# Optimization experiments

Hardware: AMD Instinct MI355X
Metric: run time of the kernel (lower is better)

## Reference

```python
import jax, jax.numpy as jnp
import numpy as np

T, B, S = 64, 128, 128
H = 200   # hidden_size
E = 200   # embedding_size
A = 100   # attention projection width
V = 10003 # vocab_size


def setup_inputs() -> dict:
    key = jax.random.key(0)
    ks = jax.random.split(key, 20)
    def n(k, shape, scale):
        return (jax.random.normal(k, shape, jnp.float32) * scale).astype(jnp.float32)
    return {
        "tokens": jax.random.randint(ks[0], (T, B), 0, V),
        "hidden": n(ks[1], (1, B, H), 0.1),
        "encoder_outputs": n(ks[2], (S, B, H), 1.0),
        "emb": n(ks[3], (V, E), 0.05),
        "W1": n(ks[4], (A, H), 0.07), "b1": n(ks[5], (A,), 0.07),
        "W2": n(ks[6], (A, H), 0.07), "b2": n(ks[7], (A,), 0.07),
        "W3": n(ks[8], (A, E), 0.07), "b3": n(ks[9], (A,), 0.07),
        "attn_W": n(ks[10], (1, A), 0.1), "attn_b": n(ks[11], (1,), 0.1),
        "gru_Wih": n(ks[12], (3 * H, E + H), 0.05), "gru_Whh": n(ks[13], (3 * H, H), 0.05),
        "gru_bih": n(ks[14], (3 * H,), 0.05), "gru_bhh": n(ks[15], (3 * H,), 0.05),
        "out_W": n(ks[16], (V, H), 0.05), "out_b": n(ks[17], (V,), 0.05),
    }


def reference(tokens, hidden, encoder_outputs, emb, W1, b1, W2, b2, W3, b3,
              attn_W, attn_b, gru_Wih, gru_Whh, gru_bih, gru_bhh, out_W, out_b):
    # eval mode: dropout is identity
    enc = jnp.transpose(encoder_outputs, (1, 0, 2))   # [B, S, H]
    embedded = emb[tokens]                            # [T, B, E]
    ah3 = embedded @ W3.T + b3                        # [T, B, A] (precomputed, as in torch)
    ah2 = enc @ W2.T + b2                             # [B, S, A]
    h0 = hidden[0]                                    # [B, H]

    def step(h, xs):
        emb_t, ah3_t = xs                             # [B,E], [B,A]
        ah1 = h @ W1.T + b1                           # [B, A]
        e = jax.nn.relu(ah1[:, None, :] + ah2 + ah3_t[:, None, :])  # [B, S, A]
        logits = (e @ attn_W.T + attn_b)[..., 0]      # [B, S]
        a = jax.nn.softmax(logits, axis=1)            # [B, S]
        ctx = jnp.einsum('bs,bsh->bh', a, enc)        # [B, H]
        x = jnp.concatenate([emb_t, ctx], axis=1)     # [B, E+H]
        gi = x @ gru_Wih.T + gru_bih                  # [B, 3H]
        gh = h @ gru_Whh.T + gru_bhh                  # [B, 3H]
        ir, iz, in_ = jnp.split(gi, 3, axis=1)
        hr, hz, hn = jnp.split(gh, 3, axis=1)
        r = jax.nn.sigmoid(ir + hr)
        z = jax.nn.sigmoid(iz + hz)
        nn_ = jnp.tanh(in_ + r * hn)
        h_new = (1.0 - z) * nn_ + z * h               # [B, H]
        logp = jax.nn.log_softmax(h_new @ out_W.T + out_b, axis=1)  # [B, V]
        return h_new, (logp, a)

    h_last, (outputs, attns) = jax.lax.scan(step, h0, (embedded, ah3))
    # outputs [T,B,V]; hidden [1,B,H]; attentions [T,B,1,S] (torch's view(B,1,S) per step)
    return outputs, h_last[None], attns[:, :, None, :]
```

## Files before the change

### kernel.cpp

```cpp
#include <hip/hip_runtime.h>
#include <hip/hip_bf16.h>
#include <cmath>

constexpr int T_ = 64, B_ = 128, S_ = 128, H_ = 200, E_ = 200, A_ = 100, V_ = 10003;
constexpr int KP = 224;
constexpr int VP = 10240;
constexpr int MROWS = T_ * B_;
constexpr int NCB = VP / 256;
constexpr int G3 = 3 * H_;
constexpr int EH = E_ + H_;
constexpr int ELD = 136;
constexpr int AH2P = 104;
constexpr int NP = 768;
constexpr int NP2 = 128;
constexpr int NTH = 512;
constexpr int NPK = 32;

typedef __attribute__((ext_vector_type(8))) short bf16x8;
typedef __attribute__((ext_vector_type(4))) float f32x4;
typedef __attribute__((ext_vector_type(2))) _Float16 h2;
typedef __attribute__((ext_vector_type(8))) _Float16 h8;

#if __has_builtin(__builtin_amdgcn_fdot2)
__device__ __forceinline__ float fdot2f(h2 a, h2 b, float c) {
  return __builtin_amdgcn_fdot2(a, b, c, false);
}
#else
__device__ __forceinline__ float fdot2f(h2 a, h2 b, float c) {
  return c + (float)a[0] * (float)b[0] + (float)a[1] * (float)b[1];
}
#endif

__device__ __forceinline__ float dot200p5(const h8* __restrict__ w, int stride,
                                          const h8* __restrict__ x) {
  const h8* p = w;
  h8 w0 = p[0]; p += stride;
  h8 w1 = p[0]; p += stride;
  h8 w2 = p[0]; p += stride;
  h8 w3 = p[0]; p += stride;
  h8 w4 = p[0]; p += stride;
  float a0 = 0.f, a1 = 0.f, a2 = 0.f, a3 = 0.f;
#define DOT_CONSUME(WREG, K)                    \
  {                                             \
    h8 xv = x[K];                               \
    h2 wp[4], xp[4];                            \
    __builtin_memcpy(wp, &WREG, 16);            \
    __builtin_memcpy(xp, &xv, 16);              \
    a0 = fdot2f(wp[0], xp[0], a0);              \
    a1 = fdot2f(wp[1], xp[1], a1);              \
    a2 = fdot2f(wp[2], xp[2], a2);              \
    a3 = fdot2f(wp[3], xp[3], a3);              \
  }
#define DOT_RELOAD(WREG) { WREG = p[0]; p += stride; }
  DOT_CONSUME(w0, 0)  DOT_RELOAD(w0)
  DOT_CONSUME(w1, 1)  DOT_RELOAD(w1)
  DOT_CONSUME(w2, 2)  DOT_RELOAD(w2)
  DOT_CONSUME(w3, 3)  DOT_RELOAD(w3)
  DOT_CONSUME(w4, 4)  DOT_RELOAD(w4)
  DOT_CONSUME(w0, 5)  DOT_RELOAD(w0)
  DOT_CONSUME(w1, 6)  DOT_RELOAD(w1)
  DOT_CONSUME(w2, 7)  DOT_RELOAD(w2)
  DOT_CONSUME(w3, 8)  DOT_RELOAD(w3)
  DOT_CONSUME(w4, 9)  DOT_RELOAD(w4)
  DOT_CONSUME(w0, 10) DOT_RELOAD(w0)
  DOT_CONSUME(w1, 11) DOT_RELOAD(w1)
  DOT_CONSUME(w2, 12) DOT_RELOAD(w2)
  DOT_CONSUME(w3, 13) DOT_RELOAD(w3)
  DOT_CONSUME(w4, 14) DOT_RELOAD(w4)
  DOT_CONSUME(w0, 15) DOT_RELOAD(w0)
  DOT_CONSUME(w1, 16) DOT_RELOAD(w1)
  DOT_CONSUME(w2, 17) DOT_RELOAD(w2)
  DOT_CONSUME(w3, 18) DOT_RELOAD(w3)
  DOT_CONSUME(w4, 19) DOT_RELOAD(w4)
  DOT_CONSUME(w0, 20)
  DOT_CONSUME(w1, 21)
  DOT_CONSUME(w2, 22)
  DOT_CONSUME(w3, 23)
  DOT_CONSUME(w4, 24)
#undef DOT_CONSUME
#undef DOT_RELOAD
  return (a0 + a1) + (a2 + a3);
}


__global__ __launch_bounds__(256) void k_pack(const float* __restrict__ W1,
                                              const float* __restrict__ Wih,
                                              const float* __restrict__ Whh,
                                              const float* __restrict__ W3,
                                              const float* __restrict__ W2,
                                              _Float16* __restrict__ W1h,
                                              _Float16* __restrict__ Wihh,
                                              _Float16* __restrict__ Whhh,
                                              __hip_bfloat16* __restrict__ wep,
                                              __hip_bfloat16* __restrict__ w2p,
                                              _Float16* __restrict__ ah2h) {
  const int stride = gridDim.x * blockDim.x;
  const int tid0 = blockIdx.x * blockDim.x + threadIdx.x;
  for (int idx = tid0; idx < 25 * A_ * 8; idx += stride) {
    int kk = idx & 7, a = (idx >> 3) % A_, k8 = idx / (8 * A_);
    W1h[idx] = (_Float16)W1[(size_t)a * H_ + k8 * 8 + kk];
  }
  for (int idx = tid0; idx < 50 * G3 * 8; idx += stride) {
    int kk = idx & 7, n = (idx >> 3) % G3, k8 = idx / (8 * G3);
    Wihh[idx] = (_Float16)Wih[(size_t)n * EH + k8 * 8 + kk];
  }
  for (int idx = tid0; idx < 25 * G3 * 8; idx += stride) {
    int kk = idx & 7, n = (idx >> 3) % G3, k8 = idx / (8 * G3);
    Whhh[idx] = (_Float16)Whh[(size_t)n * H_ + k8 * 8 + kk];
  }
  for (int idx = tid0; idx < (KP / 8) * NP * 8; idx += stride) {
    int kk = idx & 7, c = (idx >> 3) % NP, k8 = idx / (8 * NP);
    int k = k8 * 8 + kk;
    float v = 0.f;
    if (k < E_) {
      if (c < G3) v = Wih[(size_t)c * EH + k];
      else if (c < G3 + A_) v = W3[(size_t)(c - G3) * E_ + k];
    }
    wep[idx] = __float2bfloat16(v);
  }
  for (int idx = tid0; idx < (KP / 8) * NP2 * 8; idx += stride) {
    int kk = idx & 7, c = (idx >> 3) % NP2, k8 = idx / (8 * NP2);
    int k = k8 * 8 + kk;
    float v = (k < H_ && c < A_) ? W2[(size_t)c * H_ + k] : 0.f;
    w2p[idx] = __float2bfloat16(v);
  }
  for (int idx = tid0; idx < B_ * S_ * (AH2P - A_); idx += stride) {
    int row = idx / (AH2P - A_), col = A_ + idx % (AH2P - A_);
    ah2h[(size_t)row * AH2P + col] = (_Float16)0.f;
  }
}

__global__ __launch_bounds__(256) void k_genc(const float* __restrict__ encoder,
                                              const short* __restrict__ w2p,
                                              const float* __restrict__ b2,
                                              _Float16* __restrict__ ah2h) {
  constexpr int ALD = 232;
  __shared__ __align__(16) __hip_bfloat16 aL[128 * ALD];
  const int tid = threadIdx.x;
  const int w = tid >> 6, l = tid & 63, lm = l & 15, lg = l >> 4;
  const int r0 = blockIdx.y * 128;
  const int rloc = (w >> 1) * 64;
  const int v0 = (w & 1) * 64;

  for (int i = tid; i < 128 * KP; i += 256) {
    int row = i / KP, k = i - row * KP;
    float v = (k < H_) ? encoder[(size_t)(r0 + row) * H_ + k] : 0.f;
    aL[row * ALD + k] = __float2bfloat16(v);
  }
  __syncthreads();

  f32x4 acc[4][4] = {};
#pragma unroll
  for (int kt = 0; kt < KP / 32; ++kt) {
    const int k0 = kt * 32;
    bf16x8 af[4], bfr[4];
#pragma unroll
    for (int wm = 0; wm < 4; ++wm)
      af[wm] = *(const bf16x8*)(aL + (rloc + wm * 16 + lm) * ALD + k0 + lg * 8);
#pragma unroll
    for (int n = 0; n < 4; ++n)
      bfr[n] = *(const bf16x8*)(w2p + ((size_t)((k0 >> 3) + lg) * NP2 + v0 + n * 16 + lm) * 8);
#pragma unroll
    for (int wm = 0; wm < 4; ++wm)
#pragma unroll
      for (int n = 0; n < 4; ++n)
        acc[wm][n] = __builtin_amdgcn_mfma_f32_16x16x32_bf16(af[wm], bfr[n], acc[wm][n], 0, 0, 0);
  }

#pragma unroll
  for (int n = 0; n < 4; ++n) {
    const int vv = v0 + n * 16 + lm;
    if (vv >= A_) continue;
    const float bias = b2[vv];
#pragma unroll
    for (int wm = 0; wm < 4; ++wm) {
#pragma unroll
      for (int j = 0; j < 4; ++j) {
        const int grow = r0 + rloc + wm * 16 + lg * 4 + j;
        const int bb = grow & (B_ - 1);
        const int ss = grow >> 7;
        ah2h[((size_t)bb * S_ + ss) * AH2P + vv] = (_Float16)(acc[wm][n][j] + bias);
      }
    }
  }
}

__global__ __launch_bounds__(256) void k_gemb(const int* __restrict__ tokens,
                                              const float* __restrict__ emb,
                                              const short* __restrict__ wep,
                                              const float* __restrict__ bih,
                                              const float* __restrict__ b3,
                                              float* __restrict__ giX,
                                              float* __restrict__ ah3) {
  constexpr int ALD = 232;
  __shared__ __align__(16) __hip_bfloat16 aL[64 * ALD];
  __shared__ int tokL[64];
  const int tid = threadIdx.x;
  const int w = tid >> 6, l = tid & 63, lm = l & 15, lg = l >> 4;
  const int r0 = blockIdx.y * 64;
  const int v0 = blockIdx.x * 256 + w * 64;

  if (tid < 64) tokL[tid] = tokens[r0 + tid];
  __syncthreads();
  for (int i = tid; i < 64 * KP; i += 256) {
    int row = i / KP, k = i - row * KP;
    float v = (k < E_) ? emb[(size_t)tokL[row] * E_ + k] : 0.f;
    aL[row * ALD + k] = __float2bfloat16(v);
  }
  __syncthreads();

  f32x4 acc[4][4] = {};
#pragma unroll
  for (int kt = 0; kt < KP / 32; ++kt) {
    const int k0 = kt * 32;
    bf16x8 af[4], bfr[4];
#pragma unroll
    for (int wm = 0; wm < 4; ++wm)
      af[wm] = *(const bf16x8*)(aL + (wm * 16 + lm) * ALD + k0 + lg * 8);
#pragma unroll
    for (int n = 0; n < 4; ++n)
      bfr[n] = *(const bf16x8*)(wep + ((size_t)((k0 >> 3) + lg) * NP + v0 + n * 16 + lm) * 8);
#pragma unroll
    for (int wm = 0; wm < 4; ++wm)
#pragma unroll
      for (int n = 0; n < 4; ++n)
        acc[wm][n] = __builtin_amdgcn_mfma_f32_16x16x32_bf16(af[wm], bfr[n], acc[wm][n], 0, 0, 0);
  }

#pragma unroll
  for (int n = 0; n < 4; ++n) {
    const int vv = v0 + n * 16 + lm;
    const bool isGi = vv < G3;
    const bool isA3 = !isGi && vv < G3 + A_;
    const float bias = isGi ? bih[vv] : (isA3 ? b3[vv - G3] : 0.f);
#pragma unroll
    for (int wm = 0; wm < 4; ++wm) {
#pragma unroll
      for (int j = 0; j < 4; ++j) {
        const int row = r0 + wm * 16 + lg * 4 + j;
        const float val = acc[wm][n][j] + bias;
        if (isGi) giX[(size_t)row * G3 + vv] = val;
        else if (isA3) ah3[(size_t)row * A_ + (vv - G3)] = val;
      }
    }
  }
}

__global__ __launch_bounds__(NTH) void k_recur(const float* __restrict__ hidden0,
                                               const _Float16* __restrict__ ah2h,
                                               const float* __restrict__ ah3,
                                               const float* __restrict__ encoder,
                                               const _Float16* __restrict__ W1h,
                                               const float* __restrict__ b1,
                                               const float* __restrict__ attn_W,
                                               const float* __restrict__ attn_b,
                                               const _Float16* __restrict__ Wihh,
                                               const _Float16* __restrict__ Whhh,
                                               const float* __restrict__ bhh,
                                               const float* __restrict__ giX,
                                               const float* __restrict__ outW,
                                               __hip_bfloat16* __restrict__ wpk,
                                               __hip_bfloat16* __restrict__ hall,
                                               float* __restrict__ out_hidden,
                                               float* __restrict__ out_attn) {
  __shared__ __align__(16) _Float16 encLh[H_ * ELD];
  __shared__ __align__(16) h2 h16[100];
  __shared__ __align__(16) h2 xch[100];
  __shared__ __align__(16) h2 aLh[64];
  __shared__ float s1[AH2P];
  __shared__ float aW[AH2P];
  __shared__ float red[8];
  __shared__ float giL[G3];
  __shared__ float part[1200];

  const int b = blockIdx.x, tid = threadIdx.x;
  const int lane = tid & 63;

  if (b >= B_) {
    const int pt = (b - B_) * NTH + tid;
    const int pstride = NPK * NTH;
    const int total = (KP / 8) * VP * 8;
    for (int idx = pt; idx < total; idx += pstride) {
      int kk = idx & 7;
      int v = (idx >> 3) % VP;
      int kb = idx / (8 * VP);
      int k = kb * 8 + kk;
      float val = (k < H_ && v < V_) ? outW[(size_t)v * H_ + k] : 0.f;
      wpk[idx] = __float2bfloat16(val);
    }
    const __hip_bfloat16 z = __float2bfloat16(0.f);
    for (int idx = pt; idx < MROWS * (KP - H_); idx += pstride) {
      int row = idx / (KP - H_), col = H_ + idx % (KP - H_);
      hall[(size_t)row * KP + col] = z;
    }
    return;
  }

  for (int i = tid; i < S_ * H_; i += NTH) {
    int s = i / H_, h = i - s * H_;
    encLh[h * ELD + s] = (_Float16)encoder[((size_t)s * B_ + b) * H_ + h];
  }
  float hreg = 0.f, bhr = 0.f, bhz = 0.f, bhn = 0.f;
  if (tid < H_) {
    hreg = hidden0[b * H_ + tid];
    bhr = bhh[tid]; bhz = bhh[200 + tid]; bhn = bhh[400 + tid];
  }
  if (tid < 100) {
    h2 v;
    v[0] = (_Float16)hidden0[b * H_ + 2 * tid];
    v[1] = (_Float16)hidden0[b * H_ + 2 * tid + 1];
    h16[tid] = v;
  }
  for (int i = tid; i < AH2P; i += NTH) {
    aW[i] = (i < A_) ? attn_W[i] : 0.f;
    s1[i] = 0.f;
  }
  h8 ah2row[13];
  if (tid < S_) {
    const h8* src = (const h8*)(ah2h + ((size_t)b * S_ + tid) * AH2P);
#pragma unroll
    for (int r = 0; r < 13; ++r) ah2row[r] = src[r];
  }
  const float ab = attn_b[0];
  __syncthreads();

  const h8* W1h8 = (const h8*)W1h;
  const h8* Wihc8 = (const h8*)Wihh + (size_t)25 * G3;
  const h8* Whhh8 = (const h8*)Whhh;

  for (int t = 0; t < T_; ++t) {
    const h8* xs = (const h8*)h16;
    for (int u = tid; u < 700; u += NTH) {
      if (u < 100) {
        const float ah3A = ah3[((size_t)t * B_ + b) * A_ + u];
        const float b1A = b1[u];
        s1[u] = dot200p5(W1h8 + u, A_, xs) + b1A + ah3A;
      } else {
        const int g = u - 100;
        part[g] = dot200p5(Whhh8 + g, G3, xs);
      }
    }
    __syncthreads();

    float evw = 0.f;
    const int w01 = tid >> 6;
    if (tid < S_) {
      float acc = ab;
#pragma unroll
      for (int r = 0; r < 13; ++r) {
        h8 w = ah2row[r];
#pragma unroll
        for (int j = 0; j < 8; ++j) {
          const int a = r * 8 + j;
          acc += fmaxf(s1[a] + (float)w[j], 0.f) * aW[a];
        }
      }
      float m = acc;
#pragma unroll
      for (int off = 32; off > 0; off >>= 1) m = fmaxf(m, __shfl_xor(m, off, 64));
      evw = expf(acc - m);
      float sm = evw;
#pragma unroll
      for (int off = 32; off > 0; off >>= 1) sm += __shfl_xor(sm, off, 64);
      if (lane == 0) { red[w01] = m; red[4 + w01] = sm; }
    }
    __syncthreads();
    if (tid < S_) {
      const float m0 = red[0], m1 = red[1];
      const float M = fmaxf(m0, m1);
      const float SS = red[4] * expf(m0 - M) + red[5] * expf(m1 - M);
      const float av = evw * expf((w01 ? m1 : m0) - M) / SS;
      out_attn[((size_t)t * B_ + b) * S_ + tid] = av;
      const float avn = __shfl_xor(av, 1, 64);
      if ((tid & 1) == 0) {
        h2 v; v[0] = (_Float16)av; v[1] = (_Float16)avn;
        aLh[tid >> 1] = v;
      }
    }
    __syncthreads();

    if (tid < H_) {
      const h8* er = (const h8*)(encLh + tid * ELD);
      float c0 = 0.f, c1 = 0.f, c2 = 0.f, c3 = 0.f;
#pragma unroll
      for (int k8 = 0; k8 < 16; ++k8) {
        h8 evv = er[k8];
        h2 ep[4];
        __builtin_memcpy(ep, &evv, 16);
        c0 = fdot2f(ep[0], aLh[4 * k8 + 0], c0);
        c1 = fdot2f(ep[1], aLh[4 * k8 + 1], c1);
        c2 = fdot2f(ep[2], aLh[4 * k8 + 2], c2);
        c3 = fdot2f(ep[3], aLh[4 * k8 + 3], c3);
      }
      const float c = (c0 + c1) + (c2 + c3);
      const float cn = __shfl_xor(c, 1, 64);
      if ((tid & 1) == 0) {
        h2 v; v[0] = (_Float16)c; v[1] = (_Float16)cn;
        xch[tid >> 1] = v;
      }
    } else {
      const int j = tid - 200;
      if (j < 300) {
        float2 g2 = ((const float2*)(giX + ((size_t)t * B_ + b) * G3))[j];
        giL[2 * j] = g2.x;
        giL[2 * j + 1] = g2.y;
      }
    }
    __syncthreads();

    {
      const h8* xc8 = (const h8*)xch;
      for (int u = tid; u < 600; u += NTH) {
        part[600 + u] = dot200p5(Wihc8 + u, G3, xc8);
      }
    }
    __syncthreads();

    if (tid < H_) {
      const int n = tid;
      const float gir = giL[n] + part[600 + n];
      const float giz = giL[200 + n] + part[800 + n];
      const float gin = giL[400 + n] + part[1000 + n];
      const float ghr = part[n] + bhr;
      const float ghz = part[200 + n] + bhz;
      const float ghn = part[400 + n] + bhn;
      const float r = 1.f / (1.f + expf(-(gir + ghr)));
      const float z = 1.f / (1.f + expf(-(giz + ghz)));
      const float nn = tanhf(gin + r * ghn);
      const float hv = (1.f - z) * nn + z * hreg;
      hreg = hv;
      hall[((size_t)t * B_ + b) * KP + n] = __float2bfloat16(hv);
      const float hn2 = __shfl_xor(hv, 1, 64);
      if ((n & 1) == 0) {
        h2 v; v[0] = (_Float16)hv; v[1] = (_Float16)hn2;
        h16[n >> 1] = v;
      }
      if (t == T_ - 1) out_hidden[b * H_ + n] = hv;
    }
    __syncthreads();
  }
}

__global__ __launch_bounds__(256) void k_big0(const short* __restrict__ hb,
                                              const short* __restrict__ wpk,
                                              const float* __restrict__ outb,
                                              float* __restrict__ pmax,
                                              float* __restrict__ psum) {
  const int tid = threadIdx.x;
  const int w = tid >> 6, l = tid & 63;
  const int lm = l & 15, lg = l >> 4;
  const int r0 = blockIdx.y * 64;
  const int v0 = blockIdx.x * 256 + w * 64;

  f32x4 acc[4][4] = {};
#pragma unroll
  for (int kt = 0; kt < KP / 32; ++kt) {
    const int k0 = kt * 32;
    bf16x8 af[4], bfr[4];
#pragma unroll
    for (int wm = 0; wm < 4; ++wm)
      af[wm] = *(const bf16x8*)(hb + (size_t)(r0 + wm * 16 + lm) * KP + k0 + lg * 8);
#pragma unroll
    for (int n = 0; n < 4; ++n)
      bfr[n] = *(const bf16x8*)(wpk + ((size_t)((k0 >> 3) + lg) * VP + v0 + n * 16 + lm) * 8);
#pragma unroll
    for (int wm = 0; wm < 4; ++wm)
#pragma unroll
      for (int n = 0; n < 4; ++n)
        acc[wm][n] = __builtin_amdgcn_mfma_f32_16x16x32_bf16(af[wm], bfr[n], acc[wm][n], 0, 0, 0);
  }

  int vv[4]; float bias[4]; bool val[4];
#pragma unroll
  for (int n = 0; n < 4; ++n) {
    vv[n] = v0 + n * 16 + lm;
    val[n] = vv[n] < V_;
    bias[n] = val[n] ? outb[vv[n]] : 0.f;
  }

  __shared__ float smax[4][64], ssum[4][64];
#pragma unroll
  for (int wm = 0; wm < 4; ++wm) {
#pragma unroll
    for (int j = 0; j < 4; ++j) {
      float mv = -INFINITY;
#pragma unroll
      for (int n = 0; n < 4; ++n)
        if (val[n]) mv = fmaxf(mv, acc[wm][n][j] + bias[n]);
      for (int off = 8; off > 0; off >>= 1) mv = fmaxf(mv, __shfl_xor(mv, off, 64));
      float sv = 0.f;
#pragma unroll
      for (int n = 0; n < 4; ++n)
        if (val[n]) sv += expf(acc[wm][n][j] + bias[n] - mv);
      for (int off = 8; off > 0; off >>= 1) sv += __shfl_xor(sv, off, 64);
      if (lm == 0) {
        smax[w][wm * 16 + lg * 4 + j] = mv;
        ssum[w][wm * 16 + lg * 4 + j] = sv;
      }
    }
  }
  __syncthreads();
  if (tid < 64) {
    float mv = -INFINITY;
    for (int ww = 0; ww < 4; ++ww) mv = fmaxf(mv, smax[ww][tid]);
    float sv = 0.f;
    for (int ww = 0; ww < 4; ++ww) {
      float sw = ssum[ww][tid];
      if (sw > 0.f) sv += expf(smax[ww][tid] - mv) * sw;
    }
    pmax[(size_t)blockIdx.x * MROWS + r0 + tid] = mv;
    psum[(size_t)blockIdx.x * MROWS + r0 + tid] = sv;
  }
}

__global__ __launch_bounds__(256) void k_lse(const float* __restrict__ pmax,
                                             const float* __restrict__ psum,
                                             float* __restrict__ lse) {
  const int r = blockIdx.x * 256 + threadIdx.x;
  float mv = -INFINITY;
  for (int c = 0; c < NCB; ++c) mv = fmaxf(mv, pmax[(size_t)c * MROWS + r]);
  float sv = 0.f;
  for (int c = 0; c < NCB; ++c) {
    float sw = psum[(size_t)c * MROWS + r];
    if (sw > 0.f) sv += expf(pmax[(size_t)c * MROWS + r] - mv) * sw;
  }
  lse[r] = mv + logf(sv);
}

__global__ __launch_bounds__(256) void k_big1(const short* __restrict__ hb,
                                              const short* __restrict__ wpk,
                                              const float* __restrict__ outb,
                                              const float* __restrict__ lse,
                                              float* __restrict__ out_logp) {
  const int tid = threadIdx.x;
  const int w = tid >> 6, l = tid & 63;
  const int lm = l & 15, lg = l >> 4;
  const int r0 = blockIdx.y * 64;
  const int v0 = blockIdx.x * 256 + w * 64;

  __shared__ float lseL[64];
  if (tid < 64) lseL[tid] = lse[r0 + tid];

  f32x4 acc[4][4] = {};
#pragma unroll
  for (int kt = 0; kt < KP / 32; ++kt) {
    const int k0 = kt * 32;
    bf16x8 af[4], bfr[4];
#pragma unroll
    for (int wm = 0; wm < 4; ++wm)
      af[wm] = *(const bf16x8*)(hb + (size_t)(r0 + wm * 16 + lm) * KP + k0 + lg * 8);
#pragma unroll
    for (int n = 0; n < 4; ++n)
      bfr[n] = *(const bf16x8*)(wpk + ((size_t)((k0 >> 3) + lg) * VP + v0 + n * 16 + lm) * 8);
#pragma unroll
    for (int wm = 0; wm < 4; ++wm)
#pragma unroll
      for (int n = 0; n < 4; ++n)
        acc[wm][n] = __builtin_amdgcn_mfma_f32_16x16x32_bf16(af[wm], bfr[n], acc[wm][n], 0, 0, 0);
  }

  int vv[4]; float bias[4]; bool val[4];
#pragma unroll
  for (int n = 0; n < 4; ++n) {
    vv[n] = v0 + n * 16 + lm;
    val[n] = vv[n] < V_;
    bias[n] = val[n] ? outb[vv[n]] : 0.f;
  }
  __syncthreads();
#pragma unroll
  for (int wm = 0; wm < 4; ++wm) {
#pragma unroll
    for (int j = 0; j < 4; ++j) {
      const int row = r0 + wm * 16 + lg * 4 + j;
      const float ls = lseL[wm * 16 + lg * 4 + j];
#pragma unroll
      for (int n = 0; n < 4; ++n)
        if (val[n]) out_logp[(size_t)row * V_ + vv[n]] = acc[wm][n][j] + bias[n] - ls;
    }
  }
}


extern "C" void kernel_launch(void* const* d_in, const int* in_sizes, int n_in,
                              void* d_out, int out_size, void* d_ws, size_t ws_size,
                              hipStream_t stream) {
  (void)in_sizes; (void)n_in; (void)out_size; (void)ws_size;
  const int* tokens = (const int*)d_in[0];
  const float* hidden0 = (const float*)d_in[1];
  const float* encoder = (const float*)d_in[2];
  const float* emb = (const float*)d_in[3];
  const float* W1 = (const float*)d_in[4];
  const float* b1 = (const float*)d_in[5];
  const float* W2 = (const float*)d_in[6];
  const float* b2 = (const float*)d_in[7];
  const float* W3 = (const float*)d_in[8];
  const float* b3 = (const float*)d_in[9];
  const float* attn_W = (const float*)d_in[10];
  const float* attn_b = (const float*)d_in[11];
  const float* Wih = (const float*)d_in[12];
  const float* Whh = (const float*)d_in[13];
  const float* bih = (const float*)d_in[14];
  const float* bhh = (const float*)d_in[15];
  const float* outW = (const float*)d_in[16];
  const float* outb = (const float*)d_in[17];

  float* out_logp = (float*)d_out;
  float* out_hidden = out_logp + (size_t)T_ * B_ * V_;
  float* out_attn = out_hidden + (size_t)B_ * H_;

  float* ws = (float*)d_ws;
  float* ah3w = ws;
  float* pmaxw = ah3w + (size_t)T_ * B_ * A_;
  float* psumw = pmaxw + (size_t)NCB * MROWS;
  float* lsew = psumw + (size_t)NCB * MROWS;
  float* giXw = lsew + MROWS;
  __hip_bfloat16* hallw = (__hip_bfloat16*)(giXw + (size_t)MROWS * G3);
  __hip_bfloat16* wpkw = hallw + (size_t)MROWS * KP;
  _Float16* ah2hw = (_Float16*)(wpkw + (size_t)(KP / 8) * VP * 8);
  _Float16* W1hw = ah2hw + (size_t)B_ * S_ * AH2P;
  _Float16* Wihhw = W1hw + (size_t)25 * A_ * 8;
  _Float16* Whhhw = Wihhw + (size_t)50 * G3 * 8;
  __hip_bfloat16* wepw = (__hip_bfloat16*)(Whhhw + (size_t)25 * G3 * 8);
  __hip_bfloat16* w2pw = wepw + (size_t)(KP / 8) * NP * 8;

  k_pack<<<256, 256, 0, stream>>>(W1, Wih, Whh, W3, W2,
                                  W1hw, Wihhw, Whhhw, wepw, w2pw, ah2hw);
  k_genc<<<dim3(1, S_ * B_ / 128), 256, 0, stream>>>(encoder, (const short*)w2pw,
                                                     b2, ah2hw);
  k_gemb<<<dim3(NP / 256, MROWS / 64), 256, 0, stream>>>(tokens, emb, (const short*)wepw,
                                                         bih, b3, giXw, ah3w);

  k_recur<<<B_ + NPK, NTH, 0, stream>>>(hidden0, ah2hw, ah3w, encoder, W1hw, b1, attn_W,
                                        attn_b, Wihhw, Whhhw, bhh, giXw, outW, wpkw,
                                        hallw, out_hidden, out_attn);

  k_big0<<<dim3(NCB, MROWS / 64), 256, 0, stream>>>((const short*)hallw, (const short*)wpkw,
                                                    outb, pmaxw, psumw);
  k_lse<<<MROWS / 256, 256, 0, stream>>>(pmaxw, psumw, lsew);
  k_big1<<<dim3(NCB, MROWS / 64), 256, 0, stream>>>((const short*)hallw, (const short*)wpkw,
                                                    outb, lsew, out_logp);
}
```

Baseline: 996.6 us.

## Store raw logits in first pass and normalize in place instead of recomputing GEMM

The first vocab-projection kernel now writes the biased logits straight to the output while it computes per-block max and sum. The second MFMA GEMM pass is replaced by a simple elementwise kernel that subtracts the per-row log-sum-exp in place. This removes the duplicate matmul over the 10k-wide vocabulary. In exchange the roughly 330 MB output tensor is written once and then read and written again, which adds a large amount of memory traffic.

New measurement: 1.040 ms. +4.4%, slower.

```diff
diff --git a/kernel.cpp b/kernel.cpp
--- a/kernel.cpp
+++ b/kernel.cpp
@@ -445,7 +445,8 @@
                                               const short* __restrict__ wpk,
                                               const float* __restrict__ outb,
                                               float* __restrict__ pmax,
-                                              float* __restrict__ psum) {
+                                              float* __restrict__ psum,
+                                              float* __restrict__ out_logp) {
   const int tid = threadIdx.x;
   const int w = tid >> 6, l = tid & 63;
   const int lm = l & 15, lg = l >> 4;
@@ -483,6 +484,7 @@
   for (int wm = 0; wm < 4; ++wm) {
 #pragma unroll
     for (int j = 0; j < 4; ++j) {
+      const int row = r0 + wm * 16 + lg * 4 + j;
       float mv = -INFINITY;
 #pragma unroll
       for (int n = 0; n < 4; ++n)
@@ -490,8 +492,13 @@
       for (int off = 8; off > 0; off >>= 1) mv = fmaxf(mv, __shfl_xor(mv, off, 64));
       float sv = 0.f;
 #pragma unroll
-      for (int n = 0; n < 4; ++n)
-        if (val[n]) sv += expf(acc[wm][n][j] + bias[n] - mv);
+      for (int n = 0; n < 4; ++n) {
+        if (val[n]) {
+          const float lg_ = acc[wm][n][j] + bias[n];
+          sv += expf(lg_ - mv);
+          out_logp[(size_t)row * V_ + vv[n]] = lg_;
+        }
+      }
       for (int off = 8; off > 0; off >>= 1) sv += __shfl_xor(sv, off, 64);
       if (lm == 0) {
         smax[w][wm * 16 + lg * 4 + j] = mv;
@@ -527,56 +534,15 @@
   lse[r] = mv + logf(sv);
 }
 
-__global__ __launch_bounds__(256) void k_big1(const short* __restrict__ hb,
-                                              const short* __restrict__ wpk,
-                                              const float* __restrict__ outb,
-                                              const float* __restrict__ lse,
-                                              float* __restrict__ out_logp) {
-  const int tid = threadIdx.x;
-  const int w = tid >> 6, l = tid & 63;
-  const int lm = l & 15, lg = l >> 4;
-  const int r0 = blockIdx.y * 64;
-  const int v0 = blockIdx.x * 256 + w * 64;
-
-  __shared__ float lseL[64];
-  if (tid < 64) lseL[tid] = lse[r0 + tid];
-
-  f32x4 acc[4][4] = {};
-#pragma unroll
-  for (int kt = 0; kt < KP / 32; ++kt) {
-    const int k0 = kt * 32;
-    bf16x8 af[4], bfr[4];
-#pragma unroll
-    for (int wm = 0; wm < 4; ++wm)
-      af[wm] = *(const bf16x8*)(hb + (size_t)(r0 + wm * 16 + lm) * KP + k0 + lg * 8);
-#pragma unroll
-    for (int n = 0; n < 4; ++n)
-      bfr[n] = *(const bf16x8*)(wpk + ((size_t)((k0 >> 3) + lg) * VP + v0 + n * 16 + lm) * 8);
-#pragma unroll
-    for (int wm = 0; wm < 4; ++wm)
-#pragma unroll
-      for (int n = 0; n < 4; ++n)
-        acc[wm][n] = __builtin_amdgcn_mfma_f32_16x16x32_bf16(af[wm], bfr[n], acc[wm][n], 0, 0, 0);
-  }
-
-  int vv[4]; float bias[4]; bool val[4];
-#pragma unroll
-  for (int n = 0; n < 4; ++n) {
-    vv[n] = v0 + n * 16 + lm;
-    val[n] = vv[n] < V_;
-    bias[n] = val[n] ? outb[vv[n]] : 0.f;
-  }
-  __syncthreads();
-#pragma unroll
-  for (int wm = 0; wm < 4; ++wm) {
-#pragma unroll
-    for (int j = 0; j < 4; ++j) {
-      const int row = r0 + wm * 16 + lg * 4 + j;
-      const float ls = lseL[wm * 16 + lg * 4 + j];
-#pragma unroll
-      for (int n = 0; n < 4; ++n)
-        if (val[n]) out_logp[(size_t)row * V_ + vv[n]] = acc[wm][n][j] + bias[n] - ls;
-    }
+__global__ __launch_bounds__(256) void k_norm(float* __restrict__ out_logp,
+                                              const float* __restrict__ lse) {
+  const int r0 = blockIdx.x * 4;
+#pragma unroll
+  for (int rr = 0; rr < 4; ++rr) {
+    const int row = r0 + rr;
+    const float ls = lse[row];
+    float* p = out_logp + (size_t)row * V_;
+    for (int v = threadIdx.x; v < V_; v += 256) p[v] -= ls;
   }
 }
 
@@ -635,8 +601,7 @@
                                         hallw, out_hidden, out_attn);
 
   k_big0<<<dim3(NCB, MROWS / 64), 256, 0, stream>>>((const short*)hallw, (const short*)wpkw,
-                                                    outb, pmaxw, psumw);
+                                                    outb, pmaxw, psumw, out_logp);
   k_lse<<<MROWS / 256, 256, 0, stream>>>(pmaxw, psumw, lsew);
-  k_big1<<<dim3(NCB, MROWS / 64), 256, 0, stream>>>((const short*)hallw, (const short*)wpkw,
-                                                    outb, lsew, out_logp);
-}
+  k_norm<<<MROWS / 4, 256, 0, stream>>>(out_logp, lsew);
+}
```
